# Kernel optimization log

Measured on AMD Instinct MI355X. Metric: run time of the kernel, lower is better.

The kernel has to match this reference:

```python
import jax, jax.numpy as jnp
import numpy as np

B = 4
G = 1024                      # GridSize
H = 1.0 / (G - 1)             # h = (right-left)/(GridSize-1), area=[[0,0],[1,1]]
GD = 0.0                      # boundary value for hard_encode padding


def _cross(a):
    # sum of 4-neighborhood: matches conv2d with kernel [[0,.5,0],[.5,0,.5],[0,.5,0]] / 0.5
    return a[..., :-2, 1:-1] + a[..., 2:, 1:-1] + a[..., 1:-1, :-2] + a[..., 1:-1, 2:]


def _inner(a):
    return a[..., 1:-1, 1:-1]


def kappa(x, mu):
    # assumed parameterization (kappa undefined in source): exp(mu * x)
    return jnp.exp(mu * x)


def setup_inputs() -> dict:
    key = jax.random.key(0)
    k1, k2, k3, k4 = jax.random.split(key, 4)
    pre = jax.random.normal(k1, (B, 1, G - 2, G - 2), jnp.float32)
    f = jax.random.normal(k2, (B, 1, G, G), jnp.float32)
    mu = jax.random.uniform(k3, (1,), jnp.float32)
    prev_pre = jax.random.normal(k4, (B, 1, G, G), jnp.float32) * 0.1
    return {"pre": pre, "f": f, "mu": mu, "prev_pre": prev_pre, "maxiter": 20}


def reference(pre, f, mu, prev_pre, maxiter):
    # w = kappa(prev_pre, mu) is iteration-invariant -> hoist out of the loop
    w = kappa(prev_pre, mu)            # [B,1,G,G]
    w_in = _inner(w)                   # [B,1,G-2,G-2]
    force = _inner(f) * (H * H)
    # k3 conv: 0.5*cross + 2*center
    y3 = 0.5 * _cross(w) + 2.0 * w_in

    def step(y, _):
        u = jnp.pad(y, ((0, 0), (0, 0), (1, 1), (1, 1)), constant_values=GD)
        y1 = 0.5 * _cross(u) * w_in    # conv(u, k1) * w_inner
        y2 = 0.5 * _cross(w * u)       # conv(w*u, k2)
        return (force + y1 + y2) / y3, None

    # original: one jac_step, then `maxiter` more -> maxiter+1 total
    y, _ = jax.lax.scan(step, pre, None, length=maxiter + 1)
    return y
```

## Files before the change

kernel.cpp:

```cpp
#include <hip/hip_runtime.h>

#define BB 4
#define GG 1024
#define NI 1022
#define SROW 1024
#define HH2 (2.0f / (1023.0f * 1023.0f))
#define OFFC 12
#define TBR 64
#define TBC 128
#define TOUTC 104
#define NTC 10
#define HS 132

typedef float vf4 __attribute__((ext_vector_type(4)));
typedef float vf2 __attribute__((ext_vector_type(2)));

__device__ __forceinline__ float dpp_left(float x) {
    int i = __builtin_bit_cast(int, x);
    i = __builtin_amdgcn_update_dpp(i, i, 0x138, 0xf, 0xf, false);
    return __builtin_bit_cast(float, i);
}
__device__ __forceinline__ float dpp_right(float x) {
    int i = __builtin_bit_cast(int, x);
    i = __builtin_amdgcn_update_dpp(i, i, 0x130, 0xf, 0xf, false);
    return __builtin_bit_cast(float, i);
}

template<int TKP, int OFFR, int TOUTR, bool VIN4, bool VOUT4>
__global__ __launch_bounds__(512, 4)
void pinn_slab(const float* __restrict__ ysrc,
               const float* __restrict__ fglob,
               const float* __restrict__ mu_p,
               const float* __restrict__ pp,
               float* __restrict__ yout)
{
    __shared__ float ytop[2][16 * HS], ybot[2][16 * HS];
    float* const wh0 = ytop[0];
    float* const wh1 = ybot[0];

    const int tid = threadIdx.x;
    const int tx = tid & 31, ty = tid >> 5;
    const int b  = blockIdx.z;
    const int AR = blockIdx.y * TOUTR - OFFR;
    const int A0 = blockIdx.x * TOUTC - OFFC;
    const int R  = 4 * ty;
    const int c0 = 4 * tx;
    const float mu = mu_p[0];

    const int cb = min(max(A0 + c0, 0), GG - 4);
    const size_t pb = (size_t)b * GG * GG;
    const int r0 = min(max(AR + R,     0), GG - 1);
    const int r1 = min(max(AR + R + 1, 0), GG - 1);
    const int r2 = min(max(AR + R + 2, 0), GG - 1);
    const int r3 = min(max(AR + R + 3, 0), GG - 1);
    const int r4 = min(max(AR + R + 4, 0), GG - 1);
    vf4 wv0 = *(const vf4*)&pp[pb + (size_t)r0 * GG + cb];
    vf4 wv1 = *(const vf4*)&pp[pb + (size_t)r1 * GG + cb];
    vf4 wv2 = *(const vf4*)&pp[pb + (size_t)r2 * GG + cb];
    vf4 wv3 = *(const vf4*)&pp[pb + (size_t)r3 * GG + cb];
    const vf4 fv0 = *(const vf4*)&fglob[pb + (size_t)r1 * GG + cb];
    const vf4 fv1 = *(const vf4*)&fglob[pb + (size_t)r2 * GG + cb];
    const vf4 fv2 = *(const vf4*)&fglob[pb + (size_t)r3 * GG + cb];
    const vf4 fv3 = *(const vf4*)&fglob[pb + (size_t)r4 * GG + cb];

    vf4 y0v, y1v, y2v, y3v;
    {
        const int i0 = min(max(AR + R,     0), NI - 1);
        const int i1 = min(max(AR + R + 1, 0), NI - 1);
        const int i2 = min(max(AR + R + 2, 0), NI - 1);
        const int i3 = min(max(AR + R + 3, 0), NI - 1);
        if (VIN4) {
            const int cy = min(max(A0 + c0, 0), SROW - 4);
            y0v = *(const vf4*)&ysrc[(size_t)(b * NI + i0) * SROW + cy];
            y1v = *(const vf4*)&ysrc[(size_t)(b * NI + i1) * SROW + cy];
            y2v = *(const vf4*)&ysrc[(size_t)(b * NI + i2) * SROW + cy];
            y3v = *(const vf4*)&ysrc[(size_t)(b * NI + i3) * SROW + cy];
        } else {
            const int cy  = min(max(A0 + c0, 0), NI - 2);
            const int cy2 = min(cy + 2, NI - 2);
            #define LDY(dst, ii) { \
                const size_t base_ = (size_t)(b * NI + (ii)) * NI; \
                const vf2 a_ = *(const vf2*)&ysrc[base_ + cy]; \
                const vf2 b_ = *(const vf2*)&ysrc[base_ + cy2]; \
                dst[0] = a_[0]; dst[1] = a_[1]; dst[2] = b_[0]; dst[3] = b_[1]; }
            LDY(y0v, i0) LDY(y1v, i1) LDY(y2v, i2) LDY(y3v, i3)
            #undef LDY
        }
    }

    #pragma unroll
    for (int m = 0; m < 4; ++m) {
        wv0[m] = __expf(mu * wv0[m]);
        wv1[m] = __expf(mu * wv1[m]);
        wv2[m] = __expf(mu * wv2[m]);
        wv3[m] = __expf(mu * wv3[m]);
    }
    *(vf4*)&wh0[ty * HS + c0] = wv0;
    *(vf4*)&wh1[ty * HS + c0] = wv1;
    __syncthreads();

    const int nxt = min(ty + 1, 15) * HS + c0;
    const vf4 w4 = *(const vf4*)&wh0[nxt];
    const vf4 w5 = *(const vf4*)&wh1[nxt];

    const float s1_0 = dpp_right(wv0[0]);
    const float s1_1 = dpp_right(wv1[0]);
    const float s1_2 = dpp_right(wv2[0]);
    const float s1_3 = dpp_right(wv3[0]);
    const float s1_4 = dpp_right(w4[0]);
    const float s1_5 = dpp_right(w5[0]);
    const float s2_1 = dpp_right(wv1[1]);
    const float s2_2 = dpp_right(wv2[1]);
    const float s2_3 = dpp_right(wv3[1]);
    const float s2_4 = dpp_right(w4[1]);
    const float sf0 = dpp_right(fv0[0]);
    const float sf1 = dpp_right(fv1[0]);
    const float sf2 = dpp_right(fv2[0]);
    const float sf3 = dpp_right(fv3[0]);

    vf4 bN0,bN1,bN2,bN3, bS0,bS1,bS2,bS3, bW0,bW1,bW2,bW3,
        bE0,bE1,bE2,bE3, bf0,bf1,bf2,bf3;

    #define COEFF(kk, N_, C_, S_, s1N, s1C, s1S, s2C, FV, SF, BN, BS, BW, BE, BF, YV) { \
        const vf4 wN = {N_[1], N_[2], N_[3], s1N}; \
        const vf4 wW = C_; \
        const vf4 wC = {C_[1], C_[2], C_[3], s1C}; \
        const vf4 wE = {C_[2], C_[3], s1C, s2C}; \
        const vf4 wS = {S_[1], S_[2], S_[3], s1S}; \
        const vf4 aN = wC + wN, aS = wC + wS, aW = wC + wW, aE = wC + wE; \
        const vf4 den = (aN + aS) + (aW + aE); \
        const int gi = AR + R + (kk); \
        vf4 rd; \
        _Pragma("unroll") \
        for (int m = 0; m < 4; ++m) { \
            float x = __builtin_amdgcn_rcpf(den[m]); \
            x = x * (2.0f - den[m] * x); \
            const int gj = A0 + c0 + m; \
            const bool in = (gi >= 0) && (gi < NI) && (gj >= 0) && (gj < NI); \
            rd[m] = in ? x : 0.0f; \
            YV[m] = in ? YV[m] : 0.0f; \
        } \
        BN = aN * rd; BS = aS * rd; BW = aW * rd; BE = aE * rd; \
        const vf4 fC = {FV[1], FV[2], FV[3], SF}; \
        BF = (fC * rd) * HH2; }

    COEFF(0, wv0, wv1, wv2, s1_0, s1_1, s1_2, s2_1, fv0, sf0, bN0,bS0,bW0,bE0,bf0, y0v)
    COEFF(1, wv1, wv2, wv3, s1_1, s1_2, s1_3, s2_2, fv1, sf1, bN1,bS1,bW1,bE1,bf1, y1v)
    COEFF(2, wv2, wv3, w4,  s1_2, s1_3, s1_4, s2_3, fv2, sf2, bN2,bS2,bW2,bE2,bf2, y2v)
    COEFF(3, wv3, w4,  w5,  s1_3, s1_4, s1_5, s2_4, fv3, sf3, bN3,bS3,bW3,bE3,bf3, y3v)
    #undef COEFF

    const int tyo = ty * HS + c0;
    const int upo = max(ty - 1, 0)  * HS + c0;
    const int dno = min(ty + 1, 15) * HS + c0;

    for (int t = 1; t <= TKP; ++t) {
        float* tb = ytop[t & 1];
        float* bb = ybot[t & 1];
        *(vf4*)&tb[tyo] = y0v;
        *(vf4*)&bb[tyo] = y3v;
        __syncthreads();
        const vf4 up = *(const vf4*)&bb[upo];
        const vf4 dn = *(const vf4*)&tb[dno];
        const vf4 yW0 = {dpp_left(y0v[3]), y0v[0], y0v[1], y0v[2]};
        const vf4 yW1 = {dpp_left(y1v[3]), y1v[0], y1v[1], y1v[2]};
        const vf4 yW2 = {dpp_left(y2v[3]), y2v[0], y2v[1], y2v[2]};
        const vf4 yW3 = {dpp_left(y3v[3]), y3v[0], y3v[1], y3v[2]};
        const vf4 yE0 = {y0v[1], y0v[2], y0v[3], dpp_right(y0v[0])};
        const vf4 yE1 = {y1v[1], y1v[2], y1v[3], dpp_right(y1v[0])};
        const vf4 yE2 = {y2v[1], y2v[2], y2v[3], dpp_right(y2v[0])};
        const vf4 yE3 = {y3v[1], y3v[2], y3v[3], dpp_right(y3v[0])};
        vf4 n0 = bf0; n0 += bN0 * up;  n0 += bS0 * y1v; n0 += bW0 * yW0; n0 += bE0 * yE0;
        vf4 n1 = bf1; n1 += bN1 * y0v; n1 += bS1 * y2v; n1 += bW1 * yW1; n1 += bE1 * yE1;
        vf4 n2 = bf2; n2 += bN2 * y1v; n2 += bS2 * y3v; n2 += bW2 * yW2; n2 += bE2 * yE2;
        vf4 n3 = bf3; n3 += bN3 * y2v; n3 += bS3 * dn;  n3 += bW3 * yW3; n3 += bE3 * yE3;
        y0v = n0; y1v = n1; y2v = n2; y3v = n3;
    }

    if (c0 >= OFFC && c0 < OFFC + TOUTC) {
        const int gj0 = A0 + c0;
        if (VOUT4) {
            #define STORE4(kk, YV) { \
                const int r = R + (kk); \
                if (r >= OFFR && r < OFFR + TOUTR) { \
                    const int gi = AR + r; \
                    if (gi < NI && gj0 <= SROW - 4) \
                        *(vf4*)&yout[(size_t)(b * NI + gi) * SROW + gj0] = YV; } }
            STORE4(0, y0v) STORE4(1, y1v) STORE4(2, y2v) STORE4(3, y3v)
            #undef STORE4
        } else {
            #define STORE(kk, YV) { \
                const int r = R + (kk); \
                if (r >= OFFR && r < OFFR + TOUTR) { \
                    const int gi = AR + r; \
                    if (gi < NI) { \
                        const size_t rb = (size_t)(b * NI + gi) * NI; \
                        if (gj0 + 3 < NI) { \
                            vf2 pa, pv; pa[0]=YV[0]; pa[1]=YV[1]; pv[0]=YV[2]; pv[1]=YV[3]; \
                            *(vf2*)&yout[rb + gj0] = pa; *(vf2*)&yout[rb + gj0 + 2] = pv; \
                        } else { \
                            _Pragma("unroll") \
                            for (int m = 0; m < 4; ++m) \
                                if (gj0 + m < NI) yout[rb + gj0 + m] = YV[m]; \
                        } \
                    } } }
            STORE(0, y0v) STORE(1, y1v) STORE(2, y2v) STORE(3, y3v)
            #undef STORE
        }
    }
}

extern "C" void kernel_launch(void* const* d_in, const int* in_sizes, int n_in,
                              void* d_out, int out_size, void* d_ws, size_t ws_size,
                              hipStream_t stream) {
    const float* pre = (const float*)d_in[0];
    const float* f   = (const float*)d_in[1];
    const float* mu  = (const float*)d_in[2];
    const float* pp  = (const float*)d_in[3];

    float* yA = (float*)d_ws;

    const dim3 bs(512, 1, 1);
    pinn_slab<11, 11, 42, false, true ><<<dim3(NTC, 25, BB), bs, 0, stream>>>(pre, f, mu, pp, yA);
    pinn_slab<10, 10, 44, true,  false><<<dim3(NTC, 24, BB), bs, 0, stream>>>(yA,  f, mu, pp, (float*)d_out);
}
```

Measured before the change: 147.1 us.

## Halve rows per thread and double block size to 1024 threads

Each thread now holds 2 rows instead of 4, and blocks grow to 1024 threads (32 row-groups), so each block still covers the same 64-row slab. The w-coefficient setup now reads north and south neighbours from LDS instead of loading extra rows. The LDS halo stride drops from 132 to 128, which removes the padding. The aim is less per-thread register pressure and more occupancy. In exchange there are twice as many LDS halo exchanges per slab, larger blocks to synchronize each iteration, and possible bank conflicts without the padding.

```diff
diff --git a/kernel.cpp b/kernel.cpp
--- a/kernel.cpp
+++ b/kernel.cpp
@@ -6,11 +6,9 @@
 #define SROW 1024
 #define HH2 (2.0f / (1023.0f * 1023.0f))
 #define OFFC 12
-#define TBR 64
-#define TBC 128
 #define TOUTC 104
 #define NTC 10
-#define HS 132
+#define HS 128
 
 typedef float vf4 __attribute__((ext_vector_type(4)));
 typedef float vf2 __attribute__((ext_vector_type(2)));
@@ -27,54 +25,44 @@
 }
 
 template<int TKP, int OFFR, int TOUTR, bool VIN4, bool VOUT4>
-__global__ __launch_bounds__(512, 4)
+__global__ __launch_bounds__(1024, 8)
 void pinn_slab(const float* __restrict__ ysrc,
                const float* __restrict__ fglob,
                const float* __restrict__ mu_p,
                const float* __restrict__ pp,
                float* __restrict__ yout)
 {
-    __shared__ float ytop[2][16 * HS], ybot[2][16 * HS];
-    float* const wh0 = ytop[0];
-    float* const wh1 = ybot[0];
+    __shared__ float lds4[4][32 * HS];
+    float* const wh0 = lds4[0];
+    float* const wh1 = lds4[1];
 
     const int tid = threadIdx.x;
     const int tx = tid & 31, ty = tid >> 5;
     const int b  = blockIdx.z;
     const int AR = blockIdx.y * TOUTR - OFFR;
     const int A0 = blockIdx.x * TOUTC - OFFC;
-    const int R  = 4 * ty;
+    const int R  = 2 * ty;
     const int c0 = 4 * tx;
     const float mu = mu_p[0];
 
     const int cb = min(max(A0 + c0, 0), GG - 4);
     const size_t pb = (size_t)b * GG * GG;
-    const int r0 = min(max(AR + R,     0), GG - 1);
-    const int r1 = min(max(AR + R + 1, 0), GG - 1);
-    const int r2 = min(max(AR + R + 2, 0), GG - 1);
-    const int r3 = min(max(AR + R + 3, 0), GG - 1);
-    const int r4 = min(max(AR + R + 4, 0), GG - 1);
-    vf4 wv0 = *(const vf4*)&pp[pb + (size_t)r0 * GG + cb];
-    vf4 wv1 = *(const vf4*)&pp[pb + (size_t)r1 * GG + cb];
-    vf4 wv2 = *(const vf4*)&pp[pb + (size_t)r2 * GG + cb];
-    vf4 wv3 = *(const vf4*)&pp[pb + (size_t)r3 * GG + cb];
-    const vf4 fv0 = *(const vf4*)&fglob[pb + (size_t)r1 * GG + cb];
-    const vf4 fv1 = *(const vf4*)&fglob[pb + (size_t)r2 * GG + cb];
-    const vf4 fv2 = *(const vf4*)&fglob[pb + (size_t)r3 * GG + cb];
-    const vf4 fv3 = *(const vf4*)&fglob[pb + (size_t)r4 * GG + cb];
+    const int X  = AR + R;
+    const int p1 = min(max(X + 1, 0), GG - 1);
+    const int p2 = min(max(X + 2, 0), GG - 1);
+    vf4 wc0 = *(const vf4*)&pp[pb + (size_t)p1 * GG + cb];
+    vf4 wc1 = *(const vf4*)&pp[pb + (size_t)p2 * GG + cb];
+    const vf4 fv0 = *(const vf4*)&fglob[pb + (size_t)p1 * GG + cb];
+    const vf4 fv1 = *(const vf4*)&fglob[pb + (size_t)p2 * GG + cb];
 
-    vf4 y0v, y1v, y2v, y3v;
+    vf4 y0v, y1v;
     {
-        const int i0 = min(max(AR + R,     0), NI - 1);
-        const int i1 = min(max(AR + R + 1, 0), NI - 1);
-        const int i2 = min(max(AR + R + 2, 0), NI - 1);
-        const int i3 = min(max(AR + R + 3, 0), NI - 1);
+        const int i0 = min(max(X,     0), NI - 1);
+        const int i1 = min(max(X + 1, 0), NI - 1);
         if (VIN4) {
             const int cy = min(max(A0 + c0, 0), SROW - 4);
             y0v = *(const vf4*)&ysrc[(size_t)(b * NI + i0) * SROW + cy];
             y1v = *(const vf4*)&ysrc[(size_t)(b * NI + i1) * SROW + cy];
-            y2v = *(const vf4*)&ysrc[(size_t)(b * NI + i2) * SROW + cy];
-            y3v = *(const vf4*)&ysrc[(size_t)(b * NI + i3) * SROW + cy];
         } else {
             const int cy  = min(max(A0 + c0, 0), NI - 2);
             const int cy2 = min(cy + 2, NI - 2);
@@ -83,53 +71,45 @@
                 const vf2 a_ = *(const vf2*)&ysrc[base_ + cy]; \
                 const vf2 b_ = *(const vf2*)&ysrc[base_ + cy2]; \
                 dst[0] = a_[0]; dst[1] = a_[1]; dst[2] = b_[0]; dst[3] = b_[1]; }
-            LDY(y0v, i0) LDY(y1v, i1) LDY(y2v, i2) LDY(y3v, i3)
+            LDY(y0v, i0) LDY(y1v, i1)
             #undef LDY
         }
     }
 
     #pragma unroll
     for (int m = 0; m < 4; ++m) {
-        wv0[m] = __expf(mu * wv0[m]);
-        wv1[m] = __expf(mu * wv1[m]);
-        wv2[m] = __expf(mu * wv2[m]);
-        wv3[m] = __expf(mu * wv3[m]);
+        wc0[m] = __expf(mu * wc0[m]);
+        wc1[m] = __expf(mu * wc1[m]);
     }
-    *(vf4*)&wh0[ty * HS + c0] = wv0;
-    *(vf4*)&wh1[ty * HS + c0] = wv1;
+    *(vf4*)&wh0[ty * HS + c0] = wc0;
+    *(vf4*)&wh1[ty * HS + c0] = wc1;
     __syncthreads();
 
-    const int nxt = min(ty + 1, 15) * HS + c0;
-    const vf4 w4 = *(const vf4*)&wh0[nxt];
-    const vf4 w5 = *(const vf4*)&wh1[nxt];
+    const int prv = max(ty - 1, 0)  * HS + c0;
+    const int nxt = min(ty + 1, 31) * HS + c0;
+    const vf4 wN = *(const vf4*)&wh1[prv];
+    const vf4 wS = *(const vf4*)&wh0[nxt];
 
-    const float s1_0 = dpp_right(wv0[0]);
-    const float s1_1 = dpp_right(wv1[0]);
-    const float s1_2 = dpp_right(wv2[0]);
-    const float s1_3 = dpp_right(wv3[0]);
-    const float s1_4 = dpp_right(w4[0]);
-    const float s1_5 = dpp_right(w5[0]);
-    const float s2_1 = dpp_right(wv1[1]);
-    const float s2_2 = dpp_right(wv2[1]);
-    const float s2_3 = dpp_right(wv3[1]);
-    const float s2_4 = dpp_right(w4[1]);
-    const float sf0 = dpp_right(fv0[0]);
-    const float sf1 = dpp_right(fv1[0]);
-    const float sf2 = dpp_right(fv2[0]);
-    const float sf3 = dpp_right(fv3[0]);
+    const float s1N  = dpp_right(wN[0]);
+    const float s1c0 = dpp_right(wc0[0]);
+    const float s1c1 = dpp_right(wc1[0]);
+    const float s1S  = dpp_right(wS[0]);
+    const float s2c0 = dpp_right(wc0[1]);
+    const float s2c1 = dpp_right(wc1[1]);
+    const float sf0  = dpp_right(fv0[0]);
+    const float sf1  = dpp_right(fv1[0]);
 
-    vf4 bN0,bN1,bN2,bN3, bS0,bS1,bS2,bS3, bW0,bW1,bW2,bW3,
-        bE0,bE1,bE2,bE3, bf0,bf1,bf2,bf3;
+    vf4 bN0,bS0,bW0,bE0,bf0, bN1,bS1,bW1,bE1,bf1;
 
-    #define COEFF(kk, N_, C_, S_, s1N, s1C, s1S, s2C, FV, SF, BN, BS, BW, BE, BF, YV) { \
-        const vf4 wN = {N_[1], N_[2], N_[3], s1N}; \
-        const vf4 wW = C_; \
-        const vf4 wC = {C_[1], C_[2], C_[3], s1C}; \
-        const vf4 wE = {C_[2], C_[3], s1C, s2C}; \
-        const vf4 wS = {S_[1], S_[2], S_[3], s1S}; \
-        const vf4 aN = wC + wN, aS = wC + wS, aW = wC + wW, aE = wC + wE; \
+    #define COEFF(kk, N_, C_, S_, s1N_, s1C_, s1S_, s2C_, FV, SF, BN, BS, BW, BE, BF, YV) { \
+        const vf4 wNl = {N_[1], N_[2], N_[3], s1N_}; \
+        const vf4 wWl = C_; \
+        const vf4 wCl = {C_[1], C_[2], C_[3], s1C_}; \
+        const vf4 wEl = {C_[2], C_[3], s1C_, s2C_}; \
+        const vf4 wSl = {S_[1], S_[2], S_[3], s1S_}; \
+        const vf4 aN = wCl + wNl, aS = wCl + wSl, aW = wCl + wWl, aE = wCl + wEl; \
         const vf4 den = (aN + aS) + (aW + aE); \
-        const int gi = AR + R + (kk); \
+        const int gi = X + (kk); \
         vf4 rd; \
         _Pragma("unroll") \
         for (int m = 0; m < 4; ++m) { \
@@ -144,37 +124,29 @@
         const vf4 fC = {FV[1], FV[2], FV[3], SF}; \
         BF = (fC * rd) * HH2; }
 
-    COEFF(0, wv0, wv1, wv2, s1_0, s1_1, s1_2, s2_1, fv0, sf0, bN0,bS0,bW0,bE0,bf0, y0v)
-    COEFF(1, wv1, wv2, wv3, s1_1, s1_2, s1_3, s2_2, fv1, sf1, bN1,bS1,bW1,bE1,bf1, y1v)
-    COEFF(2, wv2, wv3, w4,  s1_2, s1_3, s1_4, s2_3, fv2, sf2, bN2,bS2,bW2,bE2,bf2, y2v)
-    COEFF(3, wv3, w4,  w5,  s1_3, s1_4, s1_5, s2_4, fv3, sf3, bN3,bS3,bW3,bE3,bf3, y3v)
+    COEFF(0, wN,  wc0, wc1, s1N,  s1c0, s1c1, s2c0, fv0, sf0, bN0,bS0,bW0,bE0,bf0, y0v)
+    COEFF(1, wc0, wc1, wS,  s1c0, s1c1, s1S,  s2c1, fv1, sf1, bN1,bS1,bW1,bE1,bf1, y1v)
     #undef COEFF
 
     const int tyo = ty * HS + c0;
     const int upo = max(ty - 1, 0)  * HS + c0;
-    const int dno = min(ty + 1, 15) * HS + c0;
+    const int dno = min(ty + 1, 31) * HS + c0;
 
     for (int t = 1; t <= TKP; ++t) {
-        float* tb = ytop[t & 1];
-        float* bb = ybot[t & 1];
+        float* tb = lds4[2 * (t & 1)];
+        float* bb = lds4[2 * (t & 1) + 1];
         *(vf4*)&tb[tyo] = y0v;
-        *(vf4*)&bb[tyo] = y3v;
+        *(vf4*)&bb[tyo] = y1v;
         __syncthreads();
         const vf4 up = *(const vf4*)&bb[upo];
         const vf4 dn = *(const vf4*)&tb[dno];
         const vf4 yW0 = {dpp_left(y0v[3]), y0v[0], y0v[1], y0v[2]};
         const vf4 yW1 = {dpp_left(y1v[3]), y1v[0], y1v[1], y1v[2]};
-        const vf4 yW2 = {dpp_left(y2v[3]), y2v[0], y2v[1], y2v[2]};
-        const vf4 yW3 = {dpp_left(y3v[3]), y3v[0], y3v[1], y3v[2]};
         const vf4 yE0 = {y0v[1], y0v[2], y0v[3], dpp_right(y0v[0])};
         const vf4 yE1 = {y1v[1], y1v[2], y1v[3], dpp_right(y1v[0])};
-        const vf4 yE2 = {y2v[1], y2v[2], y2v[3], dpp_right(y2v[0])};
-        const vf4 yE3 = {y3v[1], y3v[2], y3v[3], dpp_right(y3v[0])};
         vf4 n0 = bf0; n0 += bN0 * up;  n0 += bS0 * y1v; n0 += bW0 * yW0; n0 += bE0 * yE0;
-        vf4 n1 = bf1; n1 += bN1 * y0v; n1 += bS1 * y2v; n1 += bW1 * yW1; n1 += bE1 * yE1;
-        vf4 n2 = bf2; n2 += bN2 * y1v; n2 += bS2 * y3v; n2 += bW2 * yW2; n2 += bE2 * yE2;
-        vf4 n3 = bf3; n3 += bN3 * y2v; n3 += bS3 * dn;  n3 += bW3 * yW3; n3 += bE3 * yE3;
-        y0v = n0; y1v = n1; y2v = n2; y3v = n3;
+        vf4 n1 = bf1; n1 += bN1 * y0v; n1 += bS1 * dn;  n1 += bW1 * yW1; n1 += bE1 * yE1;
+        y0v = n0; y1v = n1;
     }
 
     if (c0 >= OFFC && c0 < OFFC + TOUTC) {
@@ -186,7 +158,7 @@
                     const int gi = AR + r; \
                     if (gi < NI && gj0 <= SROW - 4) \
                         *(vf4*)&yout[(size_t)(b * NI + gi) * SROW + gj0] = YV; } }
-            STORE4(0, y0v) STORE4(1, y1v) STORE4(2, y2v) STORE4(3, y3v)
+            STORE4(0, y0v) STORE4(1, y1v)
             #undef STORE4
         } else {
             #define STORE(kk, YV) { \
@@ -204,7 +176,7 @@
                                 if (gj0 + m < NI) yout[rb + gj0 + m] = YV[m]; \
                         } \
                     } } }
-            STORE(0, y0v) STORE(1, y1v) STORE(2, y2v) STORE(3, y3v)
+            STORE(0, y0v) STORE(1, y1v)
             #undef STORE
         }
     }
@@ -220,7 +192,7 @@
 
     float* yA = (float*)d_ws;
 
-    const dim3 bs(512, 1, 1);
+    const dim3 bs(1024, 1, 1);
     pinn_slab<11, 11, 42, false, true ><<<dim3(NTC, 25, BB), bs, 0, stream>>>(pre, f, mu, pp, yA);
     pinn_slab<10, 10, 44, true,  false><<<dim3(NTC, 24, BB), bs, 0, stream>>>(yA,  f, mu, pp, (float*)d_out);
 }
```

New measurement: 174.3 us. 1.18x slower.
